# Kernel tuning notes

Measured on AMD Instinct MI355X. Metric: run time of the kernel, lower is better.

The kernel has to match this reference:

```python
import jax, jax.numpy as jnp
import numpy as np

NUM_GRAPHS = 1024  # fill_max for batch ids; fixed num_segments for jit


def setup_inputs() -> dict:
    key = jax.random.key(0)
    k1, k2 = jax.random.split(key)
    N, D = 1000000, 256
    x = jax.random.normal(k1, (N, D), dtype=jnp.float32)
    batch = jnp.sort(jax.random.randint(k2, (N,), 0, NUM_GRAPHS, dtype=jnp.int64))
    return {"input": x, "batch": batch}


def reference(input, batch):
    # per-node L2 norm over feature dim: [N]
    all_norms = jnp.sqrt(jnp.sum(input.astype(jnp.float32) ** 2, axis=1))
    seg = batch.astype(jnp.int32)
    # segment-reduce: sum of norms and node counts per graph, [NUM_GRAPHS]
    norm_sum = jax.ops.segment_sum(all_norms, seg, num_segments=NUM_GRAPHS)
    counts = jax.ops.segment_sum(jnp.ones_like(all_norms), seg, num_segments=NUM_GRAPHS)
    per_graph = jnp.where(counts > 0, norm_sum / counts, 0.0)
    # original loops b in range(batch.max()) -> graphs 0..max-1 only
    bmax = batch.max().astype(jnp.float32)
    mask = jnp.arange(NUM_GRAPHS, dtype=jnp.float32) < bmax
    norm_mean = jnp.sum(per_graph * mask) / (bmax + 1.0)
    # module returns input unchanged; norm_mean is the recorded statistic
    return input, norm_mean
```

## Files before the change

kernel.cpp:

```cpp
#include <hip/hip_runtime.h>

#define NUM_GRAPHS 1024
#define D 256

__global__ void activs_init_kernel(float* __restrict__ sums, float* __restrict__ cnts) {
    int i = blockIdx.x * blockDim.x + threadIdx.x;
    if (i < NUM_GRAPHS) {
        sums[i] = 0.0f;
        cnts[i] = 0.0f;
    }
}

__device__ __forceinline__ float sq4(const float4 v) {
    return v.x * v.x + v.y * v.y + v.z * v.z + v.w * v.w;
}

struct Rows {
    float4 a0, a1, a2, a3;
    float4 b0, b1, b2, b3;
};

__device__ __forceinline__ void load_rows(Rows& R, const float* __restrict__ x,
                                          int r0, int q, int l) {
    const float4* srcA = (const float4*)(x + (size_t)(r0 + q) * D);
    const float4* srcB = (const float4*)(x + (size_t)(r0 + 4 + q) * D);
    R.a0 = srcA[l];
    R.a1 = srcA[l + 16];
    R.a2 = srcA[l + 32];
    R.a3 = srcA[l + 48];
    R.b0 = srcB[l];
    R.b1 = srcB[l + 16];
    R.b2 = srcB[l + 32];
    R.b3 = srcB[l + 48];
}

__device__ __forceinline__ void store_rows(const Rows& R, float* __restrict__ out,
                                           int r0, int q, int l) {
    float4* dstA = (float4*)(out + (size_t)(r0 + q) * D);
    float4* dstB = (float4*)(out + (size_t)(r0 + 4 + q) * D);
    dstA[l]      = R.a0;
    dstA[l + 16] = R.a1;
    dstA[l + 32] = R.a2;
    dstA[l + 48] = R.a3;
    dstB[l]      = R.b0;
    dstB[l + 16] = R.b1;
    dstB[l + 32] = R.b2;
    dstB[l + 48] = R.b3;
}

__global__ __launch_bounds__(256) void activs_main_kernel(
        const float* __restrict__ x, const int* __restrict__ batch,
        float* __restrict__ out, float* __restrict__ sums,
        float* __restrict__ cnts, int N) {
    const int lane = threadIdx.x & 63;
    const int q = lane >> 4;
    const int l = lane & 15;
    const int waveId = (blockIdx.x * blockDim.x + threadIdx.x) >> 6;
    const int totalWaves = (gridDim.x * blockDim.x) >> 6;
    const int stride = totalWaves * 8;

    const int Nq = N & ~7;

    int r = waveId * 8;
    if (r < Nq) {
        Rows cur;
        load_rows(cur, x, r, q, l);
        int4 w0 = ((const int4*)(batch + r))[0];
        int4 w1 = ((const int4*)(batch + r))[1];

        while (true) {
            const int rn = r + stride;
            const bool more = (rn < Nq);
            Rows nxt;
            int4 nw0, nw1;
            if (more) {
                load_rows(nxt, x, rn, q, l);
                nw0 = ((const int4*)(batch + rn))[0];
                nw1 = ((const int4*)(batch + rn))[1];
            }

            store_rows(cur, out, r, q, l);

            float sA = sq4(cur.a0) + sq4(cur.a1) + sq4(cur.a2) + sq4(cur.a3);
            float sB = sq4(cur.b0) + sq4(cur.b1) + sq4(cur.b2) + sq4(cur.b3);
            #pragma unroll
            for (int m = 1; m <= 8; m <<= 1) {
                sA += __shfl_xor(sA, m, 64);
                sB += __shfl_xor(sB, m, 64);
            }
            sA = sqrtf(sA);
            sB = sqrtf(sB);

            const float n0 = __shfl(sA, 0, 64), n1 = __shfl(sA, 16, 64);
            const float n2 = __shfl(sA, 32, 64), n3 = __shfl(sA, 48, 64);
            const float n4 = __shfl(sB, 0, 64), n5 = __shfl(sB, 16, 64);
            const float n6 = __shfl(sB, 32, 64), n7 = __shfl(sB, 48, 64);

            if (lane == 0) {
                const float n[8] = {n0, n1, n2, n3, n4, n5, n6, n7};
                const int b[8] = {w0.x, w0.y, w0.z, w0.w, w1.x, w1.y, w1.z, w1.w};
                int seg = b[0];
                float rs = n[0], rc = 1.0f;
                #pragma unroll
                for (int k = 1; k < 8; ++k) {
                    if (b[k] == seg) { rs += n[k]; rc += 1.0f; }
                    else {
                        atomicAdd(&sums[seg], rs);
                        atomicAdd(&cnts[seg], rc);
                        seg = b[k]; rs = n[k]; rc = 1.0f;
                    }
                }
                atomicAdd(&sums[seg], rs);
                atomicAdd(&cnts[seg], rc);
            }

            if (!more) break;
            cur = nxt;
            w0 = nw0;
            w1 = nw1;
            r = rn;
        }
    }

    if (waveId == 0) {
        for (int t = Nq; t < N; ++t) {
            const float4 v = ((const float4*)(x + (size_t)t * D))[lane];
            ((float4*)(out + (size_t)t * D))[lane] = v;
            float s = sq4(v);
            #pragma unroll
            for (int m = 32; m; m >>= 1) s += __shfl_xor(s, m, 64);
            if (lane == 0) {
                atomicAdd(&sums[batch[t]], sqrtf(s));
                atomicAdd(&cnts[batch[t]], 1.0f);
            }
        }
    }
}

__global__ __launch_bounds__(1024) void activs_finalize_kernel(
        const float* __restrict__ sums, const float* __restrict__ cnts,
        const int* __restrict__ batch, int N, float* __restrict__ out_scalar) {
    __shared__ float red[16];
    const int i = threadIdx.x;
    const int lane = i & 63;
    const int w = i >> 6;

    const float bmax = (float)batch[N - 1];

    float c = cnts[i];
    float pg = (c > 0.0f) ? (sums[i] / c) : 0.0f;
    float val = (((float)i) < bmax) ? pg : 0.0f;

    #pragma unroll
    for (int m = 32; m; m >>= 1) val += __shfl_xor(val, m, 64);
    if (lane == 0) red[w] = val;
    __syncthreads();

    if (w == 0) {
        float v = (lane < 16) ? red[lane] : 0.0f;
        #pragma unroll
        for (int m = 8; m; m >>= 1) v += __shfl_xor(v, m, 64);
        if (lane == 0) out_scalar[0] = v / (bmax + 1.0f);
    }
}

extern "C" void kernel_launch(void* const* d_in, const int* in_sizes, int n_in,
                              void* d_out, int out_size, void* d_ws, size_t ws_size,
                              hipStream_t stream) {
    const float* x = (const float*)d_in[0];
    const int* batch = (const int*)d_in[1];
    float* out = (float*)d_out;

    const int N = in_sizes[1];

    float* sums = (float*)d_ws;
    float* cnts = sums + NUM_GRAPHS;

    hipLaunchKernelGGL(activs_init_kernel, dim3(4), dim3(256), 0, stream, sums, cnts);

    hipLaunchKernelGGL(activs_main_kernel, dim3(2048), dim3(256), 0, stream,
                       x, batch, out, sums, cnts, N);

    hipLaunchKernelGGL(activs_finalize_kernel, dim3(1), dim3(1024), 0, stream,
                       sums, cnts, batch, N, out + (size_t)N * D);
}
```

Before: 414.0 us.

## Split norm streaming from segment reduction with LDS-privatized atomics

Adds a two-pass path. The first kernel copies the input and writes per-row L2 norms to workspace. The second kernel reduces norms per segment using shared-memory atomics and flushes only non-empty bins to global memory. This removes the serialized lane-0 global atomics from the bandwidth-bound streaming loop, at the cost of an extra 4 MB norms round trip and one more launch. The old fused kernel is kept as a fallback when the workspace is too small.

Result: faster. 404.4 us (-2.3%).

```diff
diff --git a/kernel.cpp b/kernel.cpp
--- a/kernel.cpp
+++ b/kernel.cpp
@@ -48,7 +48,107 @@
     dstB[l + 48] = R.b3;
 }
 
-__global__ __launch_bounds__(256) void activs_main_kernel(
+__global__ __launch_bounds__(256) void activs_stream_kernel(
+        const float* __restrict__ x, float* __restrict__ out,
+        float* __restrict__ norms, int N) {
+    const int lane = threadIdx.x & 63;
+    const int q = lane >> 4;
+    const int l = lane & 15;
+    const int waveId = (blockIdx.x * blockDim.x + threadIdx.x) >> 6;
+    const int totalWaves = (gridDim.x * blockDim.x) >> 6;
+    const int stride = totalWaves * 8;
+
+    const int Nq = N & ~7;
+
+    int r = waveId * 8;
+    if (r < Nq) {
+        Rows cur;
+        load_rows(cur, x, r, q, l);
+
+        while (true) {
+            const int rn = r + stride;
+            const bool more = (rn < Nq);
+            Rows nxt;
+            if (more) load_rows(nxt, x, rn, q, l);
+
+            store_rows(cur, out, r, q, l);
+
+            float sA = sq4(cur.a0) + sq4(cur.a1) + sq4(cur.a2) + sq4(cur.a3);
+            float sB = sq4(cur.b0) + sq4(cur.b1) + sq4(cur.b2) + sq4(cur.b3);
+            #pragma unroll
+            for (int m = 1; m <= 8; m <<= 1) {
+                sA += __shfl_xor(sA, m, 64);
+                sB += __shfl_xor(sB, m, 64);
+            }
+            if (l == 0) {
+                norms[r + q] = sqrtf(sA);
+                norms[r + 4 + q] = sqrtf(sB);
+            }
+
+            if (!more) break;
+            cur = nxt;
+            r = rn;
+        }
+    }
+
+    if (waveId == 0) {
+        for (int t = Nq; t < N; ++t) {
+            const float4 v = ((const float4*)(x + (size_t)t * D))[lane];
+            ((float4*)(out + (size_t)t * D))[lane] = v;
+            float s = sq4(v);
+            #pragma unroll
+            for (int m = 32; m; m >>= 1) s += __shfl_xor(s, m, 64);
+            if (lane == 0) norms[t] = sqrtf(s);
+        }
+    }
+}
+
+__global__ __launch_bounds__(256) void activs_segred_kernel(
+        const float* __restrict__ norms, const int* __restrict__ batch,
+        float* __restrict__ sums, float* __restrict__ cnts, int N) {
+    __shared__ float lsum[NUM_GRAPHS];
+    __shared__ float lcnt[NUM_GRAPHS];
+    const int tid = threadIdx.x;
+
+    #pragma unroll
+    for (int i = tid; i < NUM_GRAPHS; i += 256) {
+        lsum[i] = 0.0f;
+        lcnt[i] = 0.0f;
+    }
+    __syncthreads();
+
+    const int base = blockIdx.x * 1024 + tid * 4;
+    if (base < N) {
+        const float4 nv = *(const float4*)(norms + base);
+        const int4 bv = *(const int4*)(batch + base);
+        const float n[4] = {nv.x, nv.y, nv.z, nv.w};
+        const int b[4] = {bv.x, bv.y, bv.z, bv.w};
+        int seg = b[0];
+        float rs = n[0], rc = 1.0f;
+        #pragma unroll
+        for (int k = 1; k < 4; ++k) {
+            if (b[k] == seg) { rs += n[k]; rc += 1.0f; }
+            else {
+                atomicAdd(&lsum[seg], rs);
+                atomicAdd(&lcnt[seg], rc);
+                seg = b[k]; rs = n[k]; rc = 1.0f;
+            }
+        }
+        atomicAdd(&lsum[seg], rs);
+        atomicAdd(&lcnt[seg], rc);
+    }
+    __syncthreads();
+
+    #pragma unroll
+    for (int i = tid; i < NUM_GRAPHS; i += 256) {
+        if (lcnt[i] != 0.0f) {
+            atomicAdd(&sums[i], lsum[i]);
+            atomicAdd(&cnts[i], lcnt[i]);
+        }
+    }
+}
+
+__global__ __launch_bounds__(256) void activs_fused_kernel(
         const float* __restrict__ x, const int* __restrict__ batch,
         float* __restrict__ out, float* __restrict__ sums,
         float* __restrict__ cnts, int N) {
@@ -58,7 +158,6 @@
     const int waveId = (blockIdx.x * blockDim.x + threadIdx.x) >> 6;
     const int totalWaves = (gridDim.x * blockDim.x) >> 6;
     const int stride = totalWaves * 8;
-
     const int Nq = N & ~7;
 
     int r = waveId * 8;
@@ -78,7 +177,6 @@
                 nw0 = ((const int4*)(batch + rn))[0];
                 nw1 = ((const int4*)(batch + rn))[1];
             }
-
             store_rows(cur, out, r, q, l);
 
             float sA = sq4(cur.a0) + sq4(cur.a1) + sq4(cur.a2) + sq4(cur.a3);
@@ -90,7 +188,6 @@
             }
             sA = sqrtf(sA);
             sB = sqrtf(sB);
-
             const float n0 = __shfl(sA, 0, 64), n1 = __shfl(sA, 16, 64);
             const float n2 = __shfl(sA, 32, 64), n3 = __shfl(sA, 48, 64);
             const float n4 = __shfl(sB, 0, 64), n5 = __shfl(sB, 16, 64);
@@ -115,13 +212,9 @@
             }
 
             if (!more) break;
-            cur = nxt;
-            w0 = nw0;
-            w1 = nw1;
-            r = rn;
-        }
-    }
-
+            cur = nxt; w0 = nw0; w1 = nw1; r = rn;
+        }
+    }
     if (waveId == 0) {
         for (int t = Nq; t < N; ++t) {
             const float4 v = ((const float4*)(x + (size_t)t * D))[lane];
@@ -173,14 +266,27 @@
 
     const int N = in_sizes[1];
 
-    float* sums = (float*)d_ws;
-    float* cnts = sums + NUM_GRAPHS;
-
-    hipLaunchKernelGGL(activs_init_kernel, dim3(4), dim3(256), 0, stream, sums, cnts);
-
-    hipLaunchKernelGGL(activs_main_kernel, dim3(2048), dim3(256), 0, stream,
-                       x, batch, out, sums, cnts, N);
-
-    hipLaunchKernelGGL(activs_finalize_kernel, dim3(1), dim3(1024), 0, stream,
-                       sums, cnts, batch, N, out + (size_t)N * D);
-}
+    const size_t need = ((size_t)N + 2 * NUM_GRAPHS) * sizeof(float);
+    if (ws_size >= need) {
+        float* norms = (float*)d_ws;
+        float* sums = norms + N;
+        float* cnts = sums + NUM_GRAPHS;
+
+        hipLaunchKernelGGL(activs_init_kernel, dim3(4), dim3(256), 0, stream, sums, cnts);
+        hipLaunchKernelGGL(activs_stream_kernel, dim3(2048), dim3(256), 0, stream,
+                           x, out, norms, N);
+        hipLaunchKernelGGL(activs_segred_kernel, dim3((N + 1023) / 1024), dim3(256),
+                           0, stream, norms, batch, sums, cnts, N);
+        hipLaunchKernelGGL(activs_finalize_kernel, dim3(1), dim3(1024), 0, stream,
+                           sums, cnts, batch, N, out + (size_t)N * D);
+    } else {
+        float* sums = (float*)d_ws;
+        float* cnts = sums + NUM_GRAPHS;
+
+        hipLaunchKernelGGL(activs_init_kernel, dim3(4), dim3(256), 0, stream, sums, cnts);
+        hipLaunchKernelGGL(activs_fused_kernel, dim3(2048), dim3(256), 0, stream,
+                           x, batch, out, sums, cnts, N);
+        hipLaunchKernelGGL(activs_finalize_kernel, dim3(1), dim3(1024), 0, stream,
+                           sums, cnts, batch, N, out + (size_t)N * D);
+    }
+}
```
